# Kernel tuning notes

Measured on AMD Instinct MI355X. Metric: run time of the kernel, lower is better.

Reference implementation:

```python
import jax, jax.numpy as jnp
import numpy as np
import math

D_MODEL = 1024
NUM_HEADS = 16
HEAD_DIM = D_MODEL // NUM_HEADS
BATCH = 2
SEQ = 2048
NEG_INF = -1000000.0  # matches torch code's -1e6 fill


def setup_inputs() -> dict:
    key = jax.random.key(0)
    ks = jax.random.split(key, 10)
    s = 1.0 / math.sqrt(D_MODEL)
    inp = {
        "X": jax.random.normal(ks[0], (BATCH, SEQ, D_MODEL), dtype=jnp.float32),
        "Wq": jax.random.uniform(ks[1], (D_MODEL, D_MODEL), minval=-s, maxval=s, dtype=jnp.float32),
        "bq": jnp.zeros((D_MODEL,), jnp.float32),
        "Wk": jax.random.uniform(ks[2], (D_MODEL, D_MODEL), minval=-s, maxval=s, dtype=jnp.float32),
        "bk": jnp.zeros((D_MODEL,), jnp.float32),
        "Wv": jax.random.uniform(ks[3], (D_MODEL, D_MODEL), minval=-s, maxval=s, dtype=jnp.float32),
        "bv": jnp.zeros((D_MODEL,), jnp.float32),
        "Wo": jax.random.uniform(ks[4], (D_MODEL, D_MODEL), minval=-s, maxval=s, dtype=jnp.float32),
        "bo": jnp.zeros((D_MODEL,), jnp.float32),
        "valid_lens": jax.random.randint(ks[5], (BATCH, NUM_HEADS), 1, SEQ + 1, dtype=jnp.int64)
        if jax.config.jax_enable_x64 else
        jax.random.randint(ks[5], (BATCH, NUM_HEADS), 1, SEQ + 1, dtype=jnp.int32),
    }
    return inp


def _split_heads(Y, B, S):
    # (B, S, D) -> (B*H, S, head_dim), matching transpose_qkv
    return Y.reshape(B, S, NUM_HEADS, HEAD_DIM).transpose(0, 2, 1, 3).reshape(B * NUM_HEADS, S, HEAD_DIM)


def reference(X, Wq, bq, Wk, bk, Wv, bv, Wo, bo, valid_lens):
    B, S, D = X.shape
    q = _split_heads(X @ Wq.T + bq, B, S)
    k = _split_heads(X @ Wk.T + bk, B, S)
    v = _split_heads(X @ Wv.T + bv, B, S)
    scores = jnp.einsum("bqd,bkd->bqk", q, k) / math.sqrt(HEAD_DIM)  # (B*H, S, S)
    # Faithful to torch code: 2-D valid_lens reshaped to (B*H,), mask over
    # the first two dims -> entire query rows j >= valid_len set to -1e6.
    row_mask = jnp.arange(S)[None, :] < valid_lens.reshape(-1)[:, None]  # (B*H, S)
    scores = jnp.where(row_mask[:, :, None], scores, NEG_INF)
    attn = jax.nn.softmax(scores, axis=-1)
    out = jnp.einsum("bqk,bkd->bqd", attn, v)  # (B*H, S, head_dim)
    out = out.reshape(B, NUM_HEADS, S, HEAD_DIM).transpose(0, 2, 1, 3).reshape(B, S, D)
    return out @ Wo.T + bo
```

## Files before the change

### kernel.cpp

```cpp
#include <hip/hip_runtime.h>

#define SQ 2048
#define DM 1024
#define NH 16
#define HD 64

typedef __bf16 bf16x8 __attribute__((ext_vector_type(8)));
typedef float f32x4 __attribute__((ext_vector_type(4)));
typedef unsigned short u16;
typedef unsigned int u32;

__device__ __forceinline__ u16 f2b(float f) {
  union { float f; u32 u; } c; c.f = f;
  return (u16)((c.u + 0x7FFFu + ((c.u >> 16) & 1u)) >> 16);
}

__device__ __forceinline__ void gll16(const void* g, void* l) {
  __builtin_amdgcn_global_load_lds(
      (const __attribute__((address_space(1))) void*)g,
      (__attribute__((address_space(3))) void*)l, 16, 0, 0);
}

__global__ void __launch_bounds__(256) conv_bf16(
    const float* __restrict__ X,
    const float* __restrict__ Wq, const float* __restrict__ Wk,
    const float* __restrict__ Wv, const float* __restrict__ Wo,
    u16* __restrict__ Xb, u16* __restrict__ Wqb, u16* __restrict__ Wkb,
    u16* __restrict__ Wvb, u16* __restrict__ Wob) {
  const size_t e = ((size_t)blockIdx.x * 256 + threadIdx.x) * 8;
  const float* src; u16* dst; size_t rel;
  if (e < 4194304u)      { src = X;  dst = Xb;  rel = e; }
  else if (e < 5242880u) { src = Wq; dst = Wqb; rel = e - 4194304u; }
  else if (e < 6291456u) { src = Wk; dst = Wkb; rel = e - 5242880u; }
  else if (e < 7340032u) { src = Wv; dst = Wvb; rel = e - 6291456u; }
  else                   { src = Wo; dst = Wob; rel = e - 7340032u; }
  float4 a = *(const float4*)(src + rel);
  float4 b = *(const float4*)(src + rel + 4);
  union { u16 h[8]; uint4 v; } o;
  o.h[0] = f2b(a.x); o.h[1] = f2b(a.y); o.h[2] = f2b(a.z); o.h[3] = f2b(a.w);
  o.h[4] = f2b(b.x); o.h[5] = f2b(b.y); o.h[6] = f2b(b.z); o.h[7] = f2b(b.w);
  *(uint4*)(dst + rel) = o.v;
}

__device__ __forceinline__ void stage128(const u16* __restrict__ A, const u16* __restrict__ B,
                                         u16* sA, u16* sB, int m0, int n0, int kt,
                                         int w, int l) {
#pragma unroll
  for (int c = 0; c < 2; ++c) {
    const int g = w * 2 + c;
    const int s = g * 64 + l;
    const int r = s >> 2, cc = s & 3;
    gll16(A + (size_t)(m0 + r) * DM + kt * 32 + cc * 8, sA + g * 512);
    gll16(B + (size_t)(n0 + r) * DM + kt * 32 + cc * 8, sB + g * 512);
  }
}

__device__ __forceinline__ void gemm_core2(const u16* __restrict__ A, const u16* __restrict__ B,
                                           u16* sA, u16* sB,
                                           int m0, int n0, f32x4 acc[4][4]) {
  const int t = threadIdx.x, l = t & 63, w = t >> 6;
  const int wr = w >> 1, wc = w & 1, lg = l >> 4, li = l & 15;

  stage128(A, B, sA, sB, m0, n0, 0, w, l);
  __syncthreads();
  int cur = 0;
  for (int kt = 0; kt < DM / 32; ++kt) {
    if (kt + 1 < DM / 32)
      stage128(A, B, sA + (cur ^ 1) * 4096, sB + (cur ^ 1) * 4096, m0, n0, kt + 1, w, l);
    bf16x8 aF[4], bF[4];
#pragma unroll
    for (int mi = 0; mi < 4; ++mi)
      aF[mi] = *(const bf16x8*)(sA + cur * 4096 + (wr * 64 + mi * 16 + li) * 32 + lg * 8);
#pragma unroll
    for (int ni = 0; ni < 4; ++ni)
      bF[ni] = *(const bf16x8*)(sB + cur * 4096 + (wc * 64 + ni * 16 + li) * 32 + lg * 8);
#pragma unroll
    for (int mi = 0; mi < 4; ++mi)
#pragma unroll
      for (int ni = 0; ni < 4; ++ni)
        acc[mi][ni] = __builtin_amdgcn_mfma_f32_16x16x32_bf16(aF[mi], bF[ni], acc[mi][ni], 0, 0, 0);
    __syncthreads();
    cur ^= 1;
  }
}

__global__ void __launch_bounds__(256) qkv_gemm(
    const u16* __restrict__ Xb, const u16* __restrict__ Wqkv,
    const float* __restrict__ bq, const float* __restrict__ bk, const float* __restrict__ bv,
    u16* __restrict__ Qb, u16* __restrict__ Kb, u16* __restrict__ Vt) {
  __shared__ u16 sA[8192];
  __shared__ u16 sB[8192];
  const int m0 = blockIdx.y * 128, n0 = blockIdx.x * 128;
  const int mode = n0 >> 10;
  const float* bias = (mode == 0) ? bq : (mode == 1) ? bk : bv;

  f32x4 acc[4][4];
  f32x4 z4 = {0.f, 0.f, 0.f, 0.f};
#pragma unroll
  for (int i = 0; i < 4; ++i)
#pragma unroll
    for (int j = 0; j < 4; ++j) acc[i][j] = z4;

  gemm_core2(Xb, Wqkv, sA, sB, m0, n0, acc);

  const int t = threadIdx.x;
  const int l = t & 63, w = t >> 6;
  const int wr = w >> 1, wc = w & 1, lg = l >> 4, li = l & 15;
#pragma unroll
  for (int mi = 0; mi < 4; ++mi) {
    const int m = m0 + wr * 64 + mi * 16 + lg * 4;
    const int b = m >> 11;
    const int s = m & 2047;
#pragma unroll
    for (int ni = 0; ni < 4; ++ni) {
      const int n = n0 + wc * 64 + ni * 16 + li;
      const int nn = n - (mode << 10);
      const int h = nn >> 6, dd = nn & 63;
      const float bia = bias[nn];
      const size_t bh = (size_t)(b * NH + h);
      if (mode == 2) {
        union { u16 h4[4]; uint2 u; } pk;
#pragma unroll
        for (int r = 0; r < 4; ++r) pk.h4[r] = f2b(acc[mi][ni][r] + bia);
        *(uint2*)(Vt + (bh * HD + dd) * SQ + s) = pk.u;
      } else {
#pragma unroll
        for (int r = 0; r < 4; ++r) {
          const float val = acc[mi][ni][r] + bia;
          const int ss = s + r;
          if (mode == 0) Qb[(bh * SQ + ss) * HD + dd] = f2b(val * 0.180336880f);
          else           Kb[(bh * SQ + ss) * HD + dd] = f2b(val);
        }
      }
    }
  }
}

__global__ void __launch_bounds__(256) out_gemm(
    const u16* __restrict__ Ag, const u16* __restrict__ Wob,
    const float* __restrict__ bo, float* __restrict__ out) {
  __shared__ u16 sA[2][2048];
  __shared__ u16 sB[2][4096];
  const int t = threadIdx.x, l = t & 63, w = t >> 6;
  const int wr = w >> 1, wc = w & 1, lg = l >> 4, li = l & 15;
  const int m0 = blockIdx.y * 64, n0 = blockIdx.x * 128;

  auto stage = [&](int buf, int kt) {
    {
      const int s = w * 64 + l;
      const int r = s >> 2, cc = s & 3;
      gll16(Ag + (size_t)(m0 + r) * DM + kt * 32 + cc * 8, &sA[buf][w * 512]);
    }
#pragma unroll
    for (int c = 0; c < 2; ++c) {
      const int g = w * 2 + c;
      const int s = g * 64 + l;
      const int r = s >> 2, cc = s & 3;
      gll16(Wob + (size_t)(n0 + r) * DM + kt * 32 + cc * 8, &sB[buf][g * 512]);
    }
  };

  f32x4 acc[2][4];
  f32x4 z4 = {0.f, 0.f, 0.f, 0.f};
#pragma unroll
  for (int i = 0; i < 2; ++i)
#pragma unroll
    for (int j = 0; j < 4; ++j) acc[i][j] = z4;

  stage(0, 0);
  __syncthreads();
  int cur = 0;
  for (int kt = 0; kt < DM / 32; ++kt) {
    if (kt + 1 < DM / 32) stage(cur ^ 1, kt + 1);
    bf16x8 aF[2], bF[4];
#pragma unroll
    for (int mi = 0; mi < 2; ++mi)
      aF[mi] = *(const bf16x8*)(&sA[cur][(wr * 32 + mi * 16 + li) * 32 + lg * 8]);
#pragma unroll
    for (int ni = 0; ni < 4; ++ni)
      bF[ni] = *(const bf16x8*)(&sB[cur][(wc * 64 + ni * 16 + li) * 32 + lg * 8]);
#pragma unroll
    for (int mi = 0; mi < 2; ++mi)
#pragma unroll
      for (int ni = 0; ni < 4; ++ni)
        acc[mi][ni] = __builtin_amdgcn_mfma_f32_16x16x32_bf16(aF[mi], bF[ni], acc[mi][ni], 0, 0, 0);
    __syncthreads();
    cur ^= 1;
  }

#pragma unroll
  for (int mi = 0; mi < 2; ++mi) {
    const int m = m0 + wr * 32 + mi * 16 + lg * 4;
#pragma unroll
    for (int ni = 0; ni < 4; ++ni) {
      const int n = n0 + wc * 64 + ni * 16 + li;
      const float bia = bo[n];
#pragma unroll
      for (int r = 0; r < 4; ++r)
        out[(size_t)(m + r) * DM + n] = acc[mi][ni][r] + bia;
    }
  }
}

__global__ void __launch_bounds__(256, 2) attn_v10(
    const u16* __restrict__ Qb, const u16* __restrict__ Kb, const u16* __restrict__ Vt,
    const int* __restrict__ vlen, u16* __restrict__ Ao) {
  __shared__ u16 sKV[4][2][4096];
  __shared__ float lpart[4][4][16];
  const int bh = blockIdx.x, qt = blockIdx.y;
  const int t = threadIdx.x, w = t >> 6, l = t & 63, lg = l >> 4, li = l & 15;
  const int vl = vlen[bh];
  const u16* Qh = Qb + (size_t)bh * SQ * HD;
  const u16* Kh = Kb + (size_t)bh * SQ * HD;
  const u16* Vh = Vt + (size_t)bh * HD * SQ;
  const int q0 = qt * 64;
  const int k0 = w * 512;

  bf16x8 qf[4][2];
#pragma unroll
  for (int g = 0; g < 4; ++g) {
    const bool mq = (q0 + g * 16 + li) >= vl;
#pragma unroll
    for (int kk = 0; kk < 2; ++kk) {
      qf[g][kk] = *(const bf16x8*)(Qh + (size_t)(q0 + g * 16 + li) * HD + kk * 32 + lg * 8);
      if (mq) {
        union { u32 u[4]; bf16x8 v; } z; z.u[0] = z.u[1] = z.u[2] = z.u[3] = 0;
        qf[g][kk] = z.v;
      }
    }
  }

  union { u16 h[8]; bf16x8 v; } onesU;
#pragma unroll
  for (int j = 0; j < 8; ++j) onesU.h[j] = 0x3F80;
  const bf16x8 ones = onesU.v;

  int kOff[4], vOff[4];
#pragma unroll
  for (int i = 0; i < 4; ++i) {
    {
      const int s = i * 64 + l, row = s >> 3, c = s & 7;
      const int csrc = c ^ (row & 7);
      const int sig = (((row >> 2) & 3) << 3) | (((row >> 4) & 1) << 2) | (row & 3);
      kOff[i] = sig * HD + csrc * 8;
    }
    {
      const int s = i * 64 + l, d = s >> 2, c = s & 3;
      const int csrc = c ^ (d & 3);
      vOff[i] = d * SQ + csrc * 8;
    }
  }

  u16* sw = &sKV[w][0][0];
  auto stage = [&](int buf, int tt) {
    const u16* kb = Kh + (size_t)(k0 + tt * 32) * HD;
    const u16* vb = Vh + (size_t)(k0 + tt * 32);
    u16* db = sw + buf * 4096;
#pragma unroll
    for (int i = 0; i < 4; ++i) gll16(kb + kOff[i], db + i * 512);
#pragma unroll
    for (int i = 0; i < 4; ++i) gll16(vb + vOff[i], db + 2048 + i * 512);
  };

  f32x4 z4 = {0.f, 0.f, 0.f, 0.f};
  f32x4 acc[4][4], lacc[4];
#pragma unroll
  for (int g = 0; g < 4; ++g) {
    lacc[g] = z4;
#pragma unroll
    for (int n2 = 0; n2 < 4; ++n2) acc[g][n2] = z4;
  }

  stage(0, 0);
  int cur = 0;
  for (int tt = 0; tt < 16; ++tt) {
    if (tt < 15) {
      stage(cur ^ 1, tt + 1);
      asm volatile("s_waitcnt vmcnt(8)" ::: "memory");
    } else {
      asm volatile("s_waitcnt vmcnt(0)" ::: "memory");
    }
    const u16* kb_ = sw + cur * 4096;
    const u16* vb_ = sw + cur * 4096 + 2048;

    bf16x8 kf[2][2], vf[4];
#pragma unroll
    for (int ni = 0; ni < 2; ++ni) {
      const int row = ni * 16 + li;
      kf[ni][0] = *(const bf16x8*)(kb_ + row * 64 + ((lg ^ (row & 7)) * 8));
      kf[ni][1] = *(const bf16x8*)(kb_ + row * 64 + (((4 + lg) ^ (row & 7)) * 8));
    }
#pragma unroll
    for (int n2 = 0; n2 < 4; ++n2) {
      const int d = n2 * 16 + li;
      vf[n2] = *(const bf16x8*)(vb_ + d * 32 + ((lg ^ (d & 3)) * 8));
    }

#pragma unroll
    for (int g = 0; g < 4; ++g) {
      f32x4 s0 = __builtin_amdgcn_mfma_f32_16x16x32_bf16(kf[0][0], qf[g][0], z4, 0, 0, 0);
      s0 = __builtin_amdgcn_mfma_f32_16x16x32_bf16(kf[0][1], qf[g][1], s0, 0, 0, 0);
      f32x4 s1 = __builtin_amdgcn_mfma_f32_16x16x32_bf16(kf[1][0], qf[g][0], z4, 0, 0, 0);
      s1 = __builtin_amdgcn_mfma_f32_16x16x32_bf16(kf[1][1], qf[g][1], s1, 0, 0, 0);

      union { __bf16 e[8]; bf16x8 v; } P;
#pragma unroll
      for (int r = 0; r < 4; ++r) {
        P.e[r]     = (__bf16)__builtin_amdgcn_exp2f(s0[r]);
        P.e[4 + r] = (__bf16)__builtin_amdgcn_exp2f(s1[r]);
      }

      lacc[g] = __builtin_amdgcn_mfma_f32_16x16x32_bf16(ones, P.v, lacc[g], 0, 0, 0);
#pragma unroll
      for (int n2 = 0; n2 < 4; ++n2)
        acc[g][n2] = __builtin_amdgcn_mfma_f32_16x16x32_bf16(vf[n2], P.v, acc[g][n2], 0, 0, 0);
    }
    cur ^= 1;
  }

  __syncthreads();
  f32x4* op = (f32x4*)&sKV[0][0][0];
#pragma unroll
  for (int g = 0; g < 4; ++g) {
#pragma unroll
    for (int n2 = 0; n2 < 4; ++n2)
      op[(((w * 4) + g) * 4 + n2) * 64 + l] = acc[g][n2];
    if (lg == 0) lpart[w][g][li] = lacc[g][0];
  }
  __syncthreads();

  const int g = w;
  const float lf = lpart[0][g][li] + lpart[1][g][li] + lpart[2][g][li] + lpart[3][g][li];
  const float inv = 1.0f / lf;
  const int b = bh >> 4, h = bh & 15;
  const size_t rowb = ((size_t)(b * SQ + q0 + g * 16 + li)) * DM + h * HD;
#pragma unroll
  for (int n2 = 0; n2 < 4; ++n2) {
    f32x4 s = op[((0 * 4 + g) * 4 + n2) * 64 + l];
    s += op[((1 * 4 + g) * 4 + n2) * 64 + l];
    s += op[((2 * 4 + g) * 4 + n2) * 64 + l];
    s += op[((3 * 4 + g) * 4 + n2) * 64 + l];
    union { __bf16 h2[4]; uint2 u; } ov;
#pragma unroll
    for (int r = 0; r < 4; ++r) ov.h2[r] = (__bf16)(s[r] * inv);
    *(uint2*)(Ao + rowb + n2 * 16 + lg * 4) = ov.u;
  }
}

extern "C" void kernel_launch(void* const* d_in, const int* in_sizes, int n_in,
                              void* d_out, int out_size, void* d_ws, size_t ws_size,
                              hipStream_t stream) {
  const float* X  = (const float*)d_in[0];
  const float* Wq = (const float*)d_in[1];
  const float* bq = (const float*)d_in[2];
  const float* Wk = (const float*)d_in[3];
  const float* bk = (const float*)d_in[4];
  const float* Wv = (const float*)d_in[5];
  const float* bv = (const float*)d_in[6];
  const float* Wo = (const float*)d_in[7];
  const float* bo = (const float*)d_in[8];
  const int* vlen = (const int*)d_in[9];

  char* ws = (char*)d_ws;
  u16* Qb  = (u16*)(ws);
  u16* Kb  = (u16*)(ws + (size_t)8388608);
  u16* Vt  = (u16*)(ws + (size_t)16777216);
  u16* Xb  = (u16*)(ws + (size_t)25165824);
  u16* Ao  = Xb;
  u16* Wqb = (u16*)(ws + (size_t)33554432);
  u16* Wkb = (u16*)(ws + (size_t)35651584);
  u16* Wvb = (u16*)(ws + (size_t)37748736);
  u16* Wob = (u16*)(ws + (size_t)39845888);

  dim3 blk(256);
  conv_bf16<<<4096, blk, 0, stream>>>(X, Wq, Wk, Wv, Wo, Xb, Wqb, Wkb, Wvb, Wob);
  qkv_gemm<<<dim3(24, 32), blk, 0, stream>>>(Xb, Wqb, bq, bk, bv, Qb, Kb, Vt);
  attn_v10<<<dim3(32, 32), blk, 0, stream>>>(Qb, Kb, Vt, vlen, Ao);
  out_gemm<<<dim3(8, 64), blk, 0, stream>>>(Ao, Wob, bo, (float*)d_out);
}
```

Baseline: 119.1 us.

## Skip fully masked query tiles using precomputed V means, swizzle GEMM grids

Query tiles lying entirely past valid_len get uniform attention over all keys, so their output equals the mean of V. A new kernel computes that mean per head, and attention blocks for those tiles write it directly instead of running the full key loop. The change also remaps GEMM block indices so that groups of eight consecutive blocks cover different output tiles, changes the V LDS swizzle, and raises wave priority around the MFMA section. The mean buffer lives in the output buffer until out_gemm overwrites it, which relies on kernel ordering on the stream.

New measurement: 124.1 us. +4.2%, slower.

```diff
diff --git a/kernel.cpp b/kernel.cpp
--- a/kernel.cpp
+++ b/kernel.cpp
@@ -42,6 +42,26 @@
   *(uint4*)(dst + rel) = o.v;
 }
 
+__global__ void __launch_bounds__(256) mean_v(
+    const u16* __restrict__ Vt, u16* __restrict__ mv) {
+  __shared__ float part[256];
+  const int bh = blockIdx.x;
+  const int t = threadIdx.x, d = t >> 2, c = t & 3;
+  const u16* row = Vt + ((size_t)bh * HD + d) * SQ + c * 512;
+  float s = 0.f;
+  for (int i = 0; i < 64; ++i) {
+    bf16x8 v = *(const bf16x8*)(row + i * 8);
+    s += ((float)v[0] + (float)v[1]) + ((float)v[2] + (float)v[3])
+       + ((float)v[4] + (float)v[5]) + ((float)v[6] + (float)v[7]);
+  }
+  part[t] = s;
+  __syncthreads();
+  if (c == 0) {
+    const float tot = (part[t] + part[t + 1]) + (part[t + 2] + part[t + 3]);
+    mv[bh * HD + d] = f2b(tot * (1.0f / 2048.0f));
+  }
+}
+
 __device__ __forceinline__ void stage128(const u16* __restrict__ A, const u16* __restrict__ B,
                                          u16* sA, u16* sB, int m0, int n0, int kt,
                                          int w, int l) {
@@ -90,7 +110,10 @@
     u16* __restrict__ Qb, u16* __restrict__ Kb, u16* __restrict__ Vt) {
   __shared__ u16 sA[8192];
   __shared__ u16 sB[8192];
-  const int m0 = blockIdx.y * 128, n0 = blockIdx.x * 128;
+  const int id = blockIdx.x;
+  const int swz = (id & 7) * 96 + (id >> 3);
+  const int bx = swz % 24, by = swz / 24;
+  const int m0 = by * 128, n0 = bx * 128;
   const int mode = n0 >> 10;
   const float* bias = (mode == 0) ? bq : (mode == 1) ? bk : bv;
 
@@ -143,7 +166,10 @@
   __shared__ u16 sB[2][4096];
   const int t = threadIdx.x, l = t & 63, w = t >> 6;
   const int wr = w >> 1, wc = w & 1, lg = l >> 4, li = l & 15;
-  const int m0 = blockIdx.y * 64, n0 = blockIdx.x * 128;
+  const int id = blockIdx.x;
+  const int swz = (id & 7) * 64 + (id >> 3);
+  const int bx = swz >> 6, by = swz & 63;
+  const int m0 = by * 64, n0 = bx * 128;
 
   auto stage = [&](int buf, int kt) {
     {
@@ -202,18 +228,30 @@
   }
 }
 
-__global__ void __launch_bounds__(256, 2) attn_v10(
+__global__ void __launch_bounds__(256, 2) attn_v11(
     const u16* __restrict__ Qb, const u16* __restrict__ Kb, const u16* __restrict__ Vt,
-    const int* __restrict__ vlen, u16* __restrict__ Ao) {
+    const int* __restrict__ vlen, const u16* __restrict__ mv, u16* __restrict__ Ao) {
   __shared__ u16 sKV[4][2][4096];
   __shared__ float lpart[4][4][16];
   const int bh = blockIdx.x, qt = blockIdx.y;
   const int t = threadIdx.x, w = t >> 6, l = t & 63, lg = l >> 4, li = l & 15;
   const int vl = vlen[bh];
+  const int q0 = qt * 64;
+  const int b = bh >> 4, h = bh & 15;
+
+  if (q0 >= vl) {
+    const size_t rowb = ((size_t)(b * SQ + q0 + w * 16 + li)) * DM + h * HD;
+#pragma unroll
+    for (int n2 = 0; n2 < 4; ++n2) {
+      const uint2 v = *(const uint2*)(mv + bh * HD + n2 * 16 + lg * 4);
+      *(uint2*)(Ao + rowb + n2 * 16 + lg * 4) = v;
+    }
+    return;
+  }
+
   const u16* Qh = Qb + (size_t)bh * SQ * HD;
   const u16* Kh = Kb + (size_t)bh * SQ * HD;
   const u16* Vh = Vt + (size_t)bh * HD * SQ;
-  const int q0 = qt * 64;
   const int k0 = w * 512;
 
   bf16x8 qf[4][2];
@@ -246,7 +284,7 @@
     }
     {
       const int s = i * 64 + l, d = s >> 2, c = s & 3;
-      const int csrc = c ^ (d & 3);
+      const int csrc = c ^ ((d >> 2) & 3);
       vOff[i] = d * SQ + csrc * 8;
     }
   }
@@ -293,9 +331,10 @@
 #pragma unroll
     for (int n2 = 0; n2 < 4; ++n2) {
       const int d = n2 * 16 + li;
-      vf[n2] = *(const bf16x8*)(vb_ + d * 32 + ((lg ^ (d & 3)) * 8));
-    }
-
+      vf[n2] = *(const bf16x8*)(vb_ + d * 32 + ((lg ^ ((d >> 2) & 3)) * 8));
+    }
+
+    __builtin_amdgcn_s_setprio(1);
 #pragma unroll
     for (int g = 0; g < 4; ++g) {
       f32x4 s0 = __builtin_amdgcn_mfma_f32_16x16x32_bf16(kf[0][0], qf[g][0], z4, 0, 0, 0);
@@ -315,6 +354,7 @@
       for (int n2 = 0; n2 < 4; ++n2)
         acc[g][n2] = __builtin_amdgcn_mfma_f32_16x16x32_bf16(vf[n2], P.v, acc[g][n2], 0, 0, 0);
     }
+    __builtin_amdgcn_s_setprio(0);
     cur ^= 1;
   }
 
@@ -332,7 +372,6 @@
   const int g = w;
   const float lf = lpart[0][g][li] + lpart[1][g][li] + lpart[2][g][li] + lpart[3][g][li];
   const float inv = 1.0f / lf;
-  const int b = bh >> 4, h = bh & 15;
   const size_t rowb = ((size_t)(b * SQ + q0 + g * 16 + li)) * DM + h * HD;
 #pragma unroll
   for (int n2 = 0; n2 < 4; ++n2) {
@@ -372,9 +411,12 @@
   u16* Wvb = (u16*)(ws + (size_t)37748736);
   u16* Wob = (u16*)(ws + (size_t)39845888);
 
+  u16* mv = (u16*)d_out;
+
   dim3 blk(256);
   conv_bf16<<<4096, blk, 0, stream>>>(X, Wq, Wk, Wv, Wo, Xb, Wqb, Wkb, Wvb, Wob);
-  qkv_gemm<<<dim3(24, 32), blk, 0, stream>>>(Xb, Wqb, bq, bk, bv, Qb, Kb, Vt);
-  attn_v10<<<dim3(32, 32), blk, 0, stream>>>(Qb, Kb, Vt, vlen, Ao);
-  out_gemm<<<dim3(8, 64), blk, 0, stream>>>(Ao, Wob, bo, (float*)d_out);
-}
+  qkv_gemm<<<768, blk, 0, stream>>>(Xb, Wqb, bq, bk, bv, Qb, Kb, Vt);
+  mean_v<<<32, blk, 0, stream>>>(Vt, mv);
+  attn_v11<<<dim3(32, 32), blk, 0, stream>>>(Qb, Kb, Vt, vlen, mv, Ao);
+  out_gemm<<<512, blk, 0, stream>>>(Ao, Wob, bo, (float*)d_out);
+}
```
